# Kernel optimization log

Measured on AMD Instinct MI355X. Metric: run time of the kernel, lower is better.

Reference implementation:

```python
import jax, jax.numpy as jnp
import numpy as np

EPS = 0.5        # epsilon
LAM1 = 1.0       # lambda_1
LAM2 = 1.0       # lambda_2
LAM3 = 0.5       # lambda_3
NLAYER = 2
N, F = 4096, 512


def setup_inputs() -> dict:
    key = jax.random.key(0)
    ks = jax.random.split(key, 7)
    feat = jax.random.normal(ks[0], (N, F), jnp.float32)
    # scale uniform adjacencies by 1/n to mimic normalized Laplacians
    adj = jax.random.uniform(ks[1], (N, N), jnp.float32) / N
    adj1 = jax.random.uniform(ks[2], (N, N), jnp.float32) / N
    y = jax.random.uniform(ks[3], (N, F), jnp.float32)
    wy = jax.random.uniform(ks[4], (F, F), jnp.float32) * 0.01
    lim = 1.0 / np.sqrt(3 * F)
    w2_w = jax.random.uniform(ks[5], (F, 3 * F), jnp.float32, -lim, lim)
    w2_b = jax.random.uniform(ks[6], (F,), jnp.float32, -lim, lim)
    return dict(feat=feat, adj=adj, adj1=adj1, y=y, wy=wy, w2_w=w2_w, w2_b=w2_b)


def _l2norm(x):
    n = jnp.sqrt(jnp.sum(x * x, axis=1, keepdims=True))
    return x / jnp.maximum(n, 1e-12)


def reference(feat, adj, adj1, y, wy, w2_w, w2_b):
    # eval mode: dropout is identity
    z1 = feat
    z2 = feat
    for _ in range(NLAYER):
        yw = y @ wy          # [n,f]
        z1w = z1 @ wy
        z2w = z2 @ wy
        # x @ wy @ wy.T @ x.T == (x@wy) @ (x@wy).T  -> n x n Gram matrices
        temp01 = yw @ yw.T
        temp02 = z1w @ z1w.T
        temp03 = z2w @ z2w.T
        temp11 = temp01 - EPS * temp02 - (1.0 - EPS) * temp03   # [n,n]
        temp12 = yw @ wy.T + (y @ wy.T) @ wy                     # [n,f]
        temp1 = jax.nn.sigmoid(temp11 @ temp12)
        y_n = feat - LAM3 * temp1

        temp21 = -temp11                                         # [n,n]
        temp24 = z1w @ wy.T + (z1 @ wy.T) @ wy                   # [n,f]
        temp2 = jax.nn.sigmoid(temp21 @ temp24)
        z1_n = adj @ z1 - EPS * (LAM3 / LAM1) * temp2

        temp34 = z2w @ wy.T + (z2 @ wy.T) @ wy                   # [n,f]
        temp3 = jax.nn.sigmoid(temp21 @ temp34)
        z2_n = adj1 @ z2 - (1.0 - EPS) * (LAM3 / LAM2) * temp3

        y, z1, z2 = y_n, z1_n, z2_n

    p = jnp.concatenate([_l2norm(y), _l2norm(z1), _l2norm(z2)], axis=1)  # [n,3f]
    logits = p @ w2_w.T + w2_b
    return jax.nn.log_softmax(logits, axis=1)
```

## Files before the change

### kernel.cpp

```cpp
#include <hip/hip_runtime.h>
#include <string.h>

typedef unsigned short u16;
typedef __bf16 bf16_t;
typedef bf16_t bf16x8 __attribute__((ext_vector_type(8)));
typedef float f32x4 __attribute__((ext_vector_type(4)));
typedef u16 u16x4 __attribute__((ext_vector_type(4)));

#define MODE_PLAIN 0
#define MODE_FUSEQT 1
#define MODE_PARTIAL 2
#define MODE_SFIN 3
#define MODE_BIASF32 4

#define SLC 2097152L

__device__ __forceinline__ float bf2f(u16 u) {
  unsigned int x = ((unsigned int)u) << 16;
  return __builtin_bit_cast(float, x);
}
__device__ __forceinline__ u16 f2bf(float f) {
  unsigned int x = __builtin_bit_cast(unsigned int, f);
  x += 0x7fffu + ((x >> 16) & 1u);
  return (u16)(x >> 16);
}

__device__ __forceinline__ void gload_lds16(const void* g, void* l) {
  __builtin_amdgcn_global_load_lds(
      (const __attribute__((address_space(1))) void*)g,
      (__attribute__((address_space(3))) void*)l, 16, 0, 0);
}

struct GemmP {
  const u16* A0; const u16* A1;
  const u16* B;  long bz;
  const float* Bf;
  int lda, ldb, K, ksl, mode;
  u16* C; int ldc;
  u16* XwT; u16* TTp; u16* Pn;
  float* Cf; long cfz; int ldcf;
  const float* Ef; const float* Up; u16* Yc;
  const float* biasf; float* Cff;
};

__global__ __launch_bounds__(256) void gemm_nt(GemmP p) {
  __shared__ u16 smem[2 * 128 * 64];
  const int tid = threadIdx.x;
  const int lane = tid & 63, wave = tid >> 6;
  const int z = blockIdx.z >> p.ksl;
  const int kc = blockIdx.z & ((1 << p.ksl) - 1);
  const long tileM = (long)blockIdx.y * 128;
  const long tileN = (long)blockIdx.x * 128;
  u16* ldsA = smem;
  u16* ldsB = smem + 128 * 64;

  const u16* A = (z == 0) ? p.A0 : p.A1;
  const u16* B = p.B + (long)z * p.bz;
  const float* Bf = p.Bf;

  const int srow = wave * 8 + (lane >> 3);
  const int ssc = lane & 7;
  long aoff[4], boff[4];
#pragma unroll
  for (int j = 0; j < 4; ++j) {
    int r = j * 32 + srow;
    int c = ssc ^ (r & 7);
    aoff[j] = ((tileM + r) * (long)p.lda + c * 8) * 2;
    boff[j] = ((tileN + r) * (long)p.ldb + c * 8) * 2;
  }
  const int frow = tid >> 4, fcol = tid & 15;

  const int r15 = lane & 15, q = lane >> 4;
  const int wm = (wave & 1) * 64, wn = (wave >> 1) * 64;

  f32x4 acc[4][4];
#pragma unroll
  for (int i = 0; i < 4; ++i)
#pragma unroll
    for (int j = 0; j < 4; ++j) { f32x4 zz = {0.f, 0.f, 0.f, 0.f}; acc[i][j] = zz; }

  const int K64 = p.K >> 6;
  const long kofs = (long)kc * K64;
  for (int kt = 0; kt < K64; ++kt) {
    const long kb = (kofs + kt) * 128;
    __syncthreads();
#pragma unroll
    for (int j = 0; j < 4; ++j)
      gload_lds16((const char*)A + aoff[j] + kb, (char*)ldsA + (j * 256 + wave * 64) * 16);
    if (Bf) {
#pragma unroll
      for (int i = 0; i < 8; ++i) {
        int r = i * 16 + frow;
        f32x4 v = *(const f32x4*)(Bf + (tileN + r) * (long)p.ldb + (kofs + kt) * 64 + fcol * 4);
        int sc = (fcol >> 1) ^ (r & 7);
        u16x4 o; o[0] = f2bf(v[0]); o[1] = f2bf(v[1]); o[2] = f2bf(v[2]); o[3] = f2bf(v[3]);
        *(u16x4*)(ldsB + (r * 8 + sc) * 8 + (fcol & 1) * 4) = o;
      }
    } else {
#pragma unroll
      for (int j = 0; j < 4; ++j)
        gload_lds16((const char*)B + boff[j] + kb, (char*)ldsB + (j * 256 + wave * 64) * 16);
    }
    __syncthreads();
#pragma unroll
    for (int ks = 0; ks < 2; ++ks) {
      bf16x8 af[4], bfr[4];
#pragma unroll
      for (int mt = 0; mt < 4; ++mt) {
        int row = wm + mt * 16 + r15;
        int sc = (ks * 4 + q) ^ (r15 & 7);
        af[mt] = *(const bf16x8*)(ldsA + (row * 8 + sc) * 8);
      }
#pragma unroll
      for (int nt = 0; nt < 4; ++nt) {
        int row = wn + nt * 16 + r15;
        int sc = (ks * 4 + q) ^ (r15 & 7);
        bfr[nt] = *(const bf16x8*)(ldsB + (row * 8 + sc) * 8);
      }
#pragma unroll
      for (int mt = 0; mt < 4; ++mt)
#pragma unroll
        for (int nt = 0; nt < 4; ++nt)
          acc[mt][nt] = __builtin_amdgcn_mfma_f32_16x16x32_bf16(af[mt], bfr[nt], acc[mt][nt], 0, 0, 0);
    }
  }

  const int mode = p.mode;
#pragma unroll
  for (int mt = 0; mt < 4; ++mt) {
#pragma unroll
    for (int nt = 0; nt < 4; ++nt) {
      long row0 = tileM + wm + mt * 16 + q * 4;
      long col = tileN + wn + nt * 16 + r15;
      if (mode == MODE_FUSEQT) {
        long bm = row0 >> 12, n0 = row0 & 4095;
        u16x4 ov;
#pragma unroll
        for (int r = 0; r < 4; ++r) ov[r] = f2bf(acc[mt][nt][r]);
        if (col < 512) {
          *(u16x4*)(p.XwT + (bm * 512 + col) * 4096 + n0) = ov;
          float s = (bm == 0) ? 1.f : -0.5f;
          u16* pn = p.Pn + n0 * 1536 + bm * 512 + col;
#pragma unroll
          for (int r = 0; r < 4; ++r) pn[(long)r * 1536] = f2bf(s * acc[mt][nt][r]);
        } else {
          *(u16x4*)(p.TTp + (bm * 512 + (col - 512)) * 4096 + n0) = ov;
        }
      } else if (mode == MODE_PARTIAL) {
        float* c = p.Cf + (long)blockIdx.z * p.cfz + row0 * p.ldcf + col;
#pragma unroll
        for (int r = 0; r < 4; ++r) c[(long)r * p.ldcf] = acc[mt][nt][r];
      } else if (mode == MODE_SFIN) {
        long b = col >> 9, f = col & 511;
#pragma unroll
        for (int r = 0; r < 4; ++r) {
          long row = row0 + r;
          float v = acc[mt][nt][r];
          float o;
          if (b == 0) {
            o = p.Ef[row * 512 + f] - 0.5f * (1.f / (1.f + __expf(-v)));
          } else {
            const float* u = p.Up + (b - 1) * 2 * SLC + row * 512 + f;
            float e = u[0] + u[SLC];
            o = e - 0.25f * (1.f / (1.f + __expf(v)));
          }
          p.Yc[b * SLC + row * 512 + f] = f2bf(o);
        }
      } else if (mode == MODE_BIASF32) {
#pragma unroll
        for (int r = 0; r < 4; ++r)
          p.Cff[(row0 + r) * 512 + col] = acc[mt][nt][r] + p.biasf[col];
      } else {
#pragma unroll
        for (int r = 0; r < 4; ++r)
          p.C[(row0 + r) * (long)p.ldc + col] = f2bf(acc[mt][nt][r]);
      }
    }
  }
}


__global__ __launch_bounds__(256) void pack_m2_k(const float* wy, u16* M2, u16* Bcat) {
  int idx = blockIdx.x * 256 + threadIdx.x;
  int i = idx >> 9, j = idx & 511;
  u16 a = f2bf(wy[idx]);
  u16 b = f2bf(wy[(long)j * 512 + i]);
  M2[(long)i * 1024 + j] = a;
  M2[(long)i * 1024 + 512 + j] = b;
  Bcat[(long)i * 512 + j] = b;
}

__global__ __launch_bounds__(256) void init_ycat_k(const float* y, const float* feat, u16* Ycat) {
  long idx = (long)blockIdx.x * 256 + threadIdx.x;
  f32x4 a = ((const f32x4*)y)[idx];
  f32x4 f = ((const f32x4*)feat)[idx];
  u16x4 ua, uf;
#pragma unroll
  for (int i = 0; i < 4; ++i) { ua[i] = f2bf(a[i]); uf[i] = f2bf(f[i]); }
  ((u16x4*)Ycat)[idx] = ua;
  ((u16x4*)Ycat)[idx + 524288] = uf;
  ((u16x4*)Ycat)[idx + 1048576] = uf;
}

__global__ __launch_bounds__(256) void cvt_adj_k(const float* a0, const float* a1, u16* dst) {
  int z = blockIdx.y;
  const float* src = z ? a1 : a0;
  long idx = (long)blockIdx.x * 256 + threadIdx.x;
  f32x4 v = ((const f32x4*)src)[idx];
  u16x4 o;
#pragma unroll
  for (int i = 0; i < 4; ++i) o[i] = f2bf(v[i]);
  ((u16x4*)(dst + (long)z * 16777216))[idx] = o;
}

__global__ __launch_bounds__(256) void transpose_k(const u16* in, u16* out, long inz, long outz) {
  __shared__ u16 t[64][68];
  const u16* src = in + (long)blockIdx.z * inz;
  u16* dst = out + (long)blockIdx.z * outz;
  int tid = threadIdx.x;
  int tr = tid >> 4, tc = (tid & 15) * 4;
  long r0 = (long)blockIdx.y * 64, c0 = (long)blockIdx.x * 64;
#pragma unroll
  for (int i = 0; i < 4; ++i) {
    int r = i * 16 + tr;
    uint2 v = *(const uint2*)(src + (r0 + r) * 512 + c0 + tc);
    t[r][tc] = (u16)(v.x & 0xffff); t[r][tc + 1] = (u16)(v.x >> 16);
    t[r][tc + 2] = (u16)(v.y & 0xffff); t[r][tc + 3] = (u16)(v.y >> 16);
  }
  __syncthreads();
#pragma unroll
  for (int i = 0; i < 4; ++i) {
    int r = i * 16 + tr;
    unsigned int a0 = t[tc + 0][r], a1 = t[tc + 1][r], a2 = t[tc + 2][r], a3 = t[tc + 3][r];
    uint2 v; v.x = a0 | (a1 << 16); v.y = a2 | (a3 << 16);
    *(uint2*)(dst + (c0 + r) * 4096 + r0 + tc) = v;
  }
}

__global__ __launch_bounds__(256) void wt_reduce_k(const float* Wp, u16* Wt) {
  long idx = (long)blockIdx.x * 256 + threadIdx.x;
  f32x4 s = ((const f32x4*)Wp)[idx];
#pragma unroll
  for (int kc = 1; kc < 4; ++kc) s += ((const f32x4*)Wp)[idx + (long)kc * 589824];
  u16x4 o;
#pragma unroll
  for (int i = 0; i < 4; ++i) o[i] = f2bf(s[i]);
  ((u16x4*)Wt)[idx] = o;
}

__device__ __forceinline__ float waveRedSum(float v) {
#pragma unroll
  for (int o = 32; o > 0; o >>= 1) v += __shfl_down(v, o, 64);
  return v;
}
__device__ __forceinline__ float waveRedMax(float v) {
#pragma unroll
  for (int o = 32; o > 0; o >>= 1) v = fmaxf(v, __shfl_down(v, o, 64));
  return v;
}

__global__ __launch_bounds__(256) void l2norm_k(const u16* Ycat, u16* pb) {
  __shared__ float red[4];
  int i = blockIdx.x, b = blockIdx.y, t = threadIdx.x;
  const u16* row = Ycat + ((long)b * 4096 + (long)i) * 512;
  unsigned int v = *(const unsigned int*)(row + 2 * t);
  float x0 = bf2f((u16)(v & 0xffff)), x1 = bf2f((u16)(v >> 16));
  float w = waveRedSum(x0 * x0 + x1 * x1);
  if ((t & 63) == 0) red[t >> 6] = w;
  __syncthreads();
  float tot = red[0] + red[1] + red[2] + red[3];
  float inv = 1.f / fmaxf(sqrtf(tot), 1e-12f);
  unsigned int o = (unsigned int)f2bf(x0 * inv) | ((unsigned int)f2bf(x1 * inv) << 16);
  *(unsigned int*)(pb + (long)i * 1536 + b * 512 + 2 * t) = o;
}

__global__ __launch_bounds__(256) void logsoftmax_k(const float* lg, float* out) {
  __shared__ float red[4];
  int i = blockIdx.x, t = threadIdx.x;
  const float* row = lg + (long)i * 512;
  float a = row[t], b2 = row[t + 256];
  float m = waveRedMax(fmaxf(a, b2));
  if ((t & 63) == 0) red[t >> 6] = m;
  __syncthreads();
  float M = fmaxf(fmaxf(red[0], red[1]), fmaxf(red[2], red[3]));
  __syncthreads();
  float w = waveRedSum(__expf(a - M) + __expf(b2 - M));
  if ((t & 63) == 0) red[t >> 6] = w;
  __syncthreads();
  float S = red[0] + red[1] + red[2] + red[3];
  float lse = M + __logf(S);
  out[(long)i * 512 + t] = a - lse;
  out[(long)i * 512 + t + 256] = b2 - lse;
}

extern "C" void kernel_launch(void* const* d_in, const int* in_sizes, int n_in,
                              void* d_out, int out_size, void* d_ws, size_t ws_size,
                              hipStream_t stream) {
  const float* feat = (const float*)d_in[0];
  const float* adj  = (const float*)d_in[1];
  const float* adj1 = (const float*)d_in[2];
  const float* y    = (const float*)d_in[3];
  const float* wy   = (const float*)d_in[4];
  const float* w2w  = (const float*)d_in[5];
  const float* w2b  = (const float*)d_in[6];
  (void)in_sizes; (void)n_in; (void)out_size; (void)ws_size;

  char* ws = (char*)d_ws;
  size_t off = 0;
  auto alloc = [&](size_t bytes) -> void* {
    void* r = ws + off; off += (bytes + 255) & ~(size_t)255; return r;
  };
  u16* M2   = (u16*)alloc(512L * 1024 * 2);
  u16* Bcat = (u16*)alloc(1024L * 512 * 2);
  u16* adjb = (u16*)alloc(2L * 4096 * 4096 * 2);
  u16* Ycat = (u16*)alloc(3L * 4096 * 512 * 2);
  u16* Pn   = (u16*)alloc(4096L * 1536 * 2);
  u16* XwT  = (u16*)alloc(3L * 512 * 4096 * 2);
  u16* TT   = (u16*)alloc(3L * 512 * 4096 * 2);
  u16* Zt   = (u16*)alloc(2L * 512 * 4096 * 2);
  u16* Wt   = (u16*)alloc(1536L * 1536 * 2);
  float* WU = (float*)alloc(4L * 1536 * 1536 * 4);
  u16* pb = XwT;
  float* logits = (float*)Zt;

  pack_m2_k<<<1024, 256, 0, stream>>>(wy, M2, Bcat);
  init_ycat_k<<<2048, 256, 0, stream>>>(y, feat, Ycat);
  cvt_adj_k<<<dim3(16384, 2), 256, 0, stream>>>(adj, adj1, adjb);

  { GemmP p = {}; p.A0 = p.A1 = M2; p.B = M2; p.lda = 1024; p.ldb = 1024; p.K = 1024;
    p.mode = MODE_PLAIN; p.C = Bcat + 512L * 512; p.ldc = 512;
    gemm_nt<<<dim3(4, 4, 1), 256, 0, stream>>>(p); }

  for (int L = 0; L < 2; ++L) {
    { GemmP p = {}; p.A0 = p.A1 = Ycat; p.B = Bcat; p.lda = 512; p.ldb = 512; p.K = 512;
      p.mode = MODE_FUSEQT; p.XwT = XwT; p.TTp = TT; p.Pn = Pn;
      gemm_nt<<<dim3(8, 96, 1), 256, 0, stream>>>(p); }
    transpose_k<<<dim3(8, 64, 2), 256, 0, stream>>>(Ycat + SLC, Zt, SLC, SLC);
    { GemmP p = {}; p.A0 = p.A1 = TT; p.B = XwT; p.lda = 4096; p.ldb = 4096;
      p.K = 1024; p.ksl = 2; p.mode = MODE_PARTIAL; p.Cf = WU; p.cfz = 2359296; p.ldcf = 1536;
      gemm_nt<<<dim3(12, 12, 4), 256, 0, stream>>>(p); }
    wt_reduce_k<<<2304, 256, 0, stream>>>(WU, Wt);
    { GemmP p = {}; p.A0 = adjb; p.A1 = adjb + 16777216L; p.B = Zt; p.bz = SLC;
      p.lda = 4096; p.ldb = 4096; p.K = 2048; p.ksl = 1;
      p.mode = MODE_PARTIAL; p.Cf = WU; p.cfz = SLC; p.ldcf = 512;
      gemm_nt<<<dim3(4, 32, 4), 256, 0, stream>>>(p); }
    { GemmP p = {}; p.A0 = p.A1 = Pn; p.B = Wt; p.lda = 1536; p.ldb = 1536; p.K = 1536;
      p.mode = MODE_SFIN; p.Ef = feat; p.Up = WU; p.Yc = Ycat;
      gemm_nt<<<dim3(12, 32, 1), 256, 0, stream>>>(p); }
  }

  l2norm_k<<<dim3(4096, 3, 1), 256, 0, stream>>>(Ycat, pb);
  { GemmP p = {}; p.A0 = p.A1 = pb; p.Bf = w2w; p.lda = 1536; p.ldb = 1536; p.K = 1536;
    p.mode = MODE_BIASF32; p.Cff = logits; p.biasf = w2b;
    gemm_nt<<<dim3(4, 32, 1), 256, 0, stream>>>(p); }
  logsoftmax_k<<<4096, 256, 0, stream>>>(logits, (float*)d_out);
}
```

Measured before the change: 650.2 us.

## Merge independent GEMMs and elementwise jobs into heterogeneous persistent-grid launches

Replaces the per-stage gemm_nt and elementwise kernels with one fused_k kernel that dispatches several independent jobs by block-id range. Adjacency conversion, Ycat init and transposes now share a launch with GEMMs, and the Wt GEMM runs unsplit alongside the adj GEMM, which removes wt_reduce. The final logits GEMM is split-K, and its partials are summed with the bias inside logsoftmax. The aim is fewer launches and better occupancy of small grids, at the cost of imbalanced mixed blocks and a longer serial K loop for Wt.

```diff
diff --git a/kernel.cpp b/kernel.cpp
--- a/kernel.cpp
+++ b/kernel.cpp
@@ -1,5 +1,4 @@
 #include <hip/hip_runtime.h>
-#include <string.h>
 
 typedef unsigned short u16;
 typedef __bf16 bf16_t;
@@ -11,7 +10,9 @@
 #define MODE_FUSEQT 1
 #define MODE_PARTIAL 2
 #define MODE_SFIN 3
-#define MODE_BIASF32 4
+#define MODE_CVT 4
+#define MODE_INIT 5
+#define MODE_TRANS 6
 
 #define SLC 2097152L
 
@@ -31,26 +32,85 @@
       (__attribute__((address_space(3))) void*)l, 16, 0, 0);
 }
 
-struct GemmP {
-  const u16* A0; const u16* A1;
-  const u16* B;  long bz;
-  const float* Bf;
-  int lda, ldb, K, ksl, mode;
-  u16* C; int ldc;
-  u16* XwT; u16* TTp; u16* Pn;
-  float* Cf; long cfz; int ldcf;
-  const float* Ef; const float* Up; u16* Yc;
-  const float* biasf; float* Cff;
+struct Job {
+  int mode, gx, gy, ksl;
+  const u16 *A0, *A1, *B; long bz;
+  const float *Bf;
+  int lda, ldb, K;
+  u16 *C; long cfz; int ldc;
+  u16 *XwT, *TTp, *Pn;
+  float *Cf; int ldcf;
+  const float *Ef, *Up; u16 *Yc;
+  const float *S0, *S1; u16 *D0;
 };
-
-__global__ __launch_bounds__(256) void gemm_nt(GemmP p) {
-  __shared__ u16 smem[2 * 128 * 64];
+struct LaunchP { Job j[3]; int s1, s2; };
+
+__device__ __forceinline__ void run_job(const Job& p, int rb, u16* smem) {
   const int tid = threadIdx.x;
+
+  if (p.mode == MODE_CVT) {
+    const float* src = (rb < 256) ? p.S0 : p.S1;
+    u16* dst = p.D0 + ((rb < 256) ? 0L : 16777216L);
+    int r = rb & 255;
+#pragma unroll 4
+    for (int i = 0; i < 64; ++i) {
+      long idx = (long)i * 65536 + r * 256 + tid;
+      f32x4 v = ((const f32x4*)src)[idx];
+      u16x4 o;
+#pragma unroll
+      for (int k = 0; k < 4; ++k) o[k] = f2bf(v[k]);
+      ((u16x4*)dst)[idx] = o;
+    }
+    return;
+  }
+  if (p.mode == MODE_INIT) {
+#pragma unroll
+    for (int i = 0; i < 8; ++i) {
+      long idx = (long)i * 65536 + rb * 256 + tid;
+      f32x4 a = ((const f32x4*)p.S0)[idx];
+      f32x4 f = ((const f32x4*)p.S1)[idx];
+      u16x4 ua, uf;
+#pragma unroll
+      for (int k = 0; k < 4; ++k) { ua[k] = f2bf(a[k]); uf[k] = f2bf(f[k]); }
+      ((u16x4*)p.D0)[idx] = ua;
+      ((u16x4*)p.D0)[idx + 524288] = uf;
+      ((u16x4*)p.D0)[idx + 1048576] = uf;
+    }
+    return;
+  }
+  if (p.mode == MODE_TRANS) {
+    u16 (*t)[68] = (u16(*)[68])smem;
+    int zi = rb >> 9, rem = rb & 511;
+    int bx = rem >> 6, by = rem & 63;
+    const u16* src = p.A0 + (long)zi * p.bz;
+    u16* dst = p.C + (long)zi * p.cfz;
+    int tr = tid >> 4, tc = (tid & 15) * 4;
+    long r0 = (long)by * 64, c0 = (long)bx * 64;
+#pragma unroll
+    for (int i = 0; i < 4; ++i) {
+      int r = i * 16 + tr;
+      uint2 v = *(const uint2*)(src + (r0 + r) * 512 + c0 + tc);
+      t[r][tc] = (u16)(v.x & 0xffff); t[r][tc + 1] = (u16)(v.x >> 16);
+      t[r][tc + 2] = (u16)(v.y & 0xffff); t[r][tc + 3] = (u16)(v.y >> 16);
+    }
+    __syncthreads();
+#pragma unroll
+    for (int i = 0; i < 4; ++i) {
+      int r = i * 16 + tr;
+      unsigned int a0 = t[tc + 0][r], a1 = t[tc + 1][r], a2 = t[tc + 2][r], a3 = t[tc + 3][r];
+      uint2 v; v.x = a0 | (a1 << 16); v.y = a2 | (a3 << 16);
+      *(uint2*)(dst + (c0 + r) * 4096 + r0 + tc) = v;
+    }
+    return;
+  }
+
   const int lane = tid & 63, wave = tid >> 6;
-  const int z = blockIdx.z >> p.ksl;
-  const int kc = blockIdx.z & ((1 << p.ksl) - 1);
-  const long tileM = (long)blockIdx.y * 128;
-  const long tileN = (long)blockIdx.x * 128;
+  int per = p.gx * p.gy;
+  int zi = rb / per, rem = rb - zi * per;
+  int bx = rem / p.gy, by = rem - bx * p.gy;
+  int z = zi >> p.ksl, kc = zi & ((1 << p.ksl) - 1);
+  const long tileM = (long)by * 128;
+  const long tileN = (long)bx * 128;
   u16* ldsA = smem;
   u16* ldsB = smem + 128 * 64;
 
@@ -147,7 +207,7 @@
           *(u16x4*)(p.TTp + (bm * 512 + (col - 512)) * 4096 + n0) = ov;
         }
       } else if (mode == MODE_PARTIAL) {
-        float* c = p.Cf + (long)blockIdx.z * p.cfz + row0 * p.ldcf + col;
+        float* c = p.Cf + (long)zi * p.cfz + row0 * p.ldcf + col;
 #pragma unroll
         for (int r = 0; r < 4; ++r) c[(long)r * p.ldcf] = acc[mt][nt][r];
       } else if (mode == MODE_SFIN) {
@@ -166,10 +226,6 @@
           }
           p.Yc[b * SLC + row * 512 + f] = f2bf(o);
         }
-      } else if (mode == MODE_BIASF32) {
-#pragma unroll
-        for (int r = 0; r < 4; ++r)
-          p.Cff[(row0 + r) * 512 + col] = acc[mt][nt][r] + p.biasf[col];
       } else {
 #pragma unroll
         for (int r = 0; r < 4; ++r)
@@ -177,6 +233,14 @@
       }
     }
   }
+}
+
+__global__ __launch_bounds__(256) void fused_k(LaunchP lp) {
+  __shared__ u16 smem[2 * 128 * 64];
+  int bid = blockIdx.x;
+  if (bid < lp.s1) run_job(lp.j[0], bid, smem);
+  else if (bid < lp.s2) run_job(lp.j[1], bid - lp.s1, smem);
+  else run_job(lp.j[2], bid - lp.s2, smem);
 }
 
 
@@ -188,64 +252,6 @@
   M2[(long)i * 1024 + j] = a;
   M2[(long)i * 1024 + 512 + j] = b;
   Bcat[(long)i * 512 + j] = b;
-}
-
-__global__ __launch_bounds__(256) void init_ycat_k(const float* y, const float* feat, u16* Ycat) {
-  long idx = (long)blockIdx.x * 256 + threadIdx.x;
-  f32x4 a = ((const f32x4*)y)[idx];
-  f32x4 f = ((const f32x4*)feat)[idx];
-  u16x4 ua, uf;
-#pragma unroll
-  for (int i = 0; i < 4; ++i) { ua[i] = f2bf(a[i]); uf[i] = f2bf(f[i]); }
-  ((u16x4*)Ycat)[idx] = ua;
-  ((u16x4*)Ycat)[idx + 524288] = uf;
-  ((u16x4*)Ycat)[idx + 1048576] = uf;
-}
-
-__global__ __launch_bounds__(256) void cvt_adj_k(const float* a0, const float* a1, u16* dst) {
-  int z = blockIdx.y;
-  const float* src = z ? a1 : a0;
-  long idx = (long)blockIdx.x * 256 + threadIdx.x;
-  f32x4 v = ((const f32x4*)src)[idx];
-  u16x4 o;
-#pragma unroll
-  for (int i = 0; i < 4; ++i) o[i] = f2bf(v[i]);
-  ((u16x4*)(dst + (long)z * 16777216))[idx] = o;
-}
-
-__global__ __launch_bounds__(256) void transpose_k(const u16* in, u16* out, long inz, long outz) {
-  __shared__ u16 t[64][68];
-  const u16* src = in + (long)blockIdx.z * inz;
-  u16* dst = out + (long)blockIdx.z * outz;
-  int tid = threadIdx.x;
-  int tr = tid >> 4, tc = (tid & 15) * 4;
-  long r0 = (long)blockIdx.y * 64, c0 = (long)blockIdx.x * 64;
-#pragma unroll
-  for (int i = 0; i < 4; ++i) {
-    int r = i * 16 + tr;
-    uint2 v = *(const uint2*)(src + (r0 + r) * 512 + c0 + tc);
-    t[r][tc] = (u16)(v.x & 0xffff); t[r][tc + 1] = (u16)(v.x >> 16);
-    t[r][tc + 2] = (u16)(v.y & 0xffff); t[r][tc + 3] = (u16)(v.y >> 16);
-  }
-  __syncthreads();
-#pragma unroll
-  for (int i = 0; i < 4; ++i) {
-    int r = i * 16 + tr;
-    unsigned int a0 = t[tc + 0][r], a1 = t[tc + 1][r], a2 = t[tc + 2][r], a3 = t[tc + 3][r];
-    uint2 v; v.x = a0 | (a1 << 16); v.y = a2 | (a3 << 16);
-    *(uint2*)(dst + (c0 + r) * 4096 + r0 + tc) = v;
-  }
-}
-
-__global__ __launch_bounds__(256) void wt_reduce_k(const float* Wp, u16* Wt) {
-  long idx = (long)blockIdx.x * 256 + threadIdx.x;
-  f32x4 s = ((const f32x4*)Wp)[idx];
-#pragma unroll
-  for (int kc = 1; kc < 4; ++kc) s += ((const f32x4*)Wp)[idx + (long)kc * 589824];
-  u16x4 o;
-#pragma unroll
-  for (int i = 0; i < 4; ++i) o[i] = f2bf(s[i]);
-  ((u16x4*)Wt)[idx] = o;
 }
 
 __device__ __forceinline__ float waveRedSum(float v) {
@@ -274,11 +280,12 @@
   *(unsigned int*)(pb + (long)i * 1536 + b * 512 + 2 * t) = o;
 }
 
-__global__ __launch_bounds__(256) void logsoftmax_k(const float* lg, float* out) {
+__global__ __launch_bounds__(256) void logsoftmax_k(const float* lg, const float* bias, float* out) {
   __shared__ float red[4];
   int i = blockIdx.x, t = threadIdx.x;
   const float* row = lg + (long)i * 512;
-  float a = row[t], b2 = row[t + 256];
+  float a  = row[t]       + row[t + SLC]       + row[t + 2 * SLC]       + row[t + 3 * SLC]       + bias[t];
+  float b2 = row[t + 256] + row[t + 256 + SLC] + row[t + 256 + 2 * SLC] + row[t + 256 + 3 * SLC] + bias[t + 256];
   float m = waveRedMax(fmaxf(a, b2));
   if ((t & 63) == 0) red[t >> 6] = m;
   __syncthreads();
@@ -319,39 +326,60 @@
   u16* TT   = (u16*)alloc(3L * 512 * 4096 * 2);
   u16* Zt   = (u16*)alloc(2L * 512 * 4096 * 2);
   u16* Wt   = (u16*)alloc(1536L * 1536 * 2);
-  float* WU = (float*)alloc(4L * 1536 * 1536 * 4);
+  float* WU = (float*)alloc(4L * SLC * 4);
   u16* pb = XwT;
-  float* logits = (float*)Zt;
 
   pack_m2_k<<<1024, 256, 0, stream>>>(wy, M2, Bcat);
-  init_ycat_k<<<2048, 256, 0, stream>>>(y, feat, Ycat);
-  cvt_adj_k<<<dim3(16384, 2), 256, 0, stream>>>(adj, adj1, adjb);
-
-  { GemmP p = {}; p.A0 = p.A1 = M2; p.B = M2; p.lda = 1024; p.ldb = 1024; p.K = 1024;
-    p.mode = MODE_PLAIN; p.C = Bcat + 512L * 512; p.ldc = 512;
-    gemm_nt<<<dim3(4, 4, 1), 256, 0, stream>>>(p); }
+
+  { LaunchP lp = {};
+    Job& a = lp.j[0]; a.mode = MODE_PLAIN; a.gx = 4; a.gy = 4; a.K = 1024;
+    a.A0 = a.A1 = M2; a.B = M2; a.lda = 1024; a.ldb = 1024;
+    a.C = Bcat + 512L * 512; a.ldc = 512;
+    Job& b = lp.j[1]; b.mode = MODE_INIT; b.S0 = y; b.S1 = feat; b.D0 = Ycat;
+    lp.s1 = 16; lp.s2 = 272;
+    fused_k<<<272, 256, 0, stream>>>(lp); }
 
   for (int L = 0; L < 2; ++L) {
-    { GemmP p = {}; p.A0 = p.A1 = Ycat; p.B = Bcat; p.lda = 512; p.ldb = 512; p.K = 512;
-      p.mode = MODE_FUSEQT; p.XwT = XwT; p.TTp = TT; p.Pn = Pn;
-      gemm_nt<<<dim3(8, 96, 1), 256, 0, stream>>>(p); }
-    transpose_k<<<dim3(8, 64, 2), 256, 0, stream>>>(Ycat + SLC, Zt, SLC, SLC);
-    { GemmP p = {}; p.A0 = p.A1 = TT; p.B = XwT; p.lda = 4096; p.ldb = 4096;
-      p.K = 1024; p.ksl = 2; p.mode = MODE_PARTIAL; p.Cf = WU; p.cfz = 2359296; p.ldcf = 1536;
-      gemm_nt<<<dim3(12, 12, 4), 256, 0, stream>>>(p); }
-    wt_reduce_k<<<2304, 256, 0, stream>>>(WU, Wt);
-    { GemmP p = {}; p.A0 = adjb; p.A1 = adjb + 16777216L; p.B = Zt; p.bz = SLC;
-      p.lda = 4096; p.ldb = 4096; p.K = 2048; p.ksl = 1;
-      p.mode = MODE_PARTIAL; p.Cf = WU; p.cfz = SLC; p.ldcf = 512;
-      gemm_nt<<<dim3(4, 32, 4), 256, 0, stream>>>(p); }
-    { GemmP p = {}; p.A0 = p.A1 = Pn; p.B = Wt; p.lda = 1536; p.ldb = 1536; p.K = 1536;
-      p.mode = MODE_SFIN; p.Ef = feat; p.Up = WU; p.Yc = Ycat;
-      gemm_nt<<<dim3(12, 32, 1), 256, 0, stream>>>(p); }
+    { LaunchP lp = {};
+      Job& a = lp.j[0]; a.mode = MODE_FUSEQT; a.gx = 8; a.gy = 96; a.K = 512;
+      a.A0 = a.A1 = Ycat; a.B = Bcat; a.lda = 512; a.ldb = 512;
+      a.XwT = XwT; a.TTp = TT; a.Pn = Pn;
+      Job& b = lp.j[1]; b.mode = MODE_TRANS; b.A0 = Ycat + SLC; b.bz = SLC;
+      b.C = Zt; b.cfz = SLC;
+      int grid = 1792;
+      lp.s1 = 768; lp.s2 = 1792;
+      if (L == 0) {
+        Job& c = lp.j[2]; c.mode = MODE_CVT; c.S0 = adj; c.S1 = adj1; c.D0 = adjb;
+        grid = 2304;
+      }
+      fused_k<<<grid, 256, 0, stream>>>(lp); }
+
+    { LaunchP lp = {};
+      Job& a = lp.j[0]; a.mode = MODE_PARTIAL; a.gx = 4; a.gy = 32; a.ksl = 1; a.K = 2048;
+      a.A0 = adjb; a.A1 = adjb + 16777216L; a.B = Zt; a.bz = SLC;
+      a.lda = 4096; a.ldb = 4096; a.Cf = WU; a.cfz = SLC; a.ldcf = 512;
+      Job& b = lp.j[1]; b.mode = MODE_PLAIN; b.gx = 12; b.gy = 12; b.K = 4096;
+      b.A0 = b.A1 = TT; b.B = XwT; b.lda = 4096; b.ldb = 4096;
+      b.C = Wt; b.ldc = 1536;
+      lp.s1 = 512; lp.s2 = 656;
+      fused_k<<<656, 256, 0, stream>>>(lp); }
+
+    { LaunchP lp = {};
+      Job& a = lp.j[0]; a.mode = MODE_SFIN; a.gx = 12; a.gy = 32; a.K = 1536;
+      a.A0 = a.A1 = Pn; a.B = Wt; a.lda = 1536; a.ldb = 1536;
+      a.Ef = feat; a.Up = WU; a.Yc = Ycat;
+      lp.s1 = 384; lp.s2 = 384;
+      fused_k<<<384, 256, 0, stream>>>(lp); }
   }
 
   l2norm_k<<<dim3(4096, 3, 1), 256, 0, stream>>>(Ycat, pb);
-  { GemmP p = {}; p.A0 = p.A1 = pb; p.Bf = w2w; p.lda = 1536; p.ldb = 1536; p.K = 1536;
-    p.mode = MODE_BIASF32; p.Cff = logits; p.biasf = w2b;
-    gemm_nt<<<dim3(4, 32, 1), 256, 0, stream>>>(p); }
-  logsoftmax_k<<<4096, 256, 0, stream>>>(logits, (float*)d_out);
-}
+
+  { LaunchP lp = {};
+    Job& a = lp.j[0]; a.mode = MODE_PARTIAL; a.gx = 4; a.gy = 32; a.ksl = 2; a.K = 384;
+    a.A0 = a.A1 = pb; a.Bf = w2w; a.lda = 1536; a.ldb = 1536;
+    a.Cf = WU; a.cfz = SLC; a.ldcf = 512;
+    lp.s1 = 512; lp.s2 = 512;
+    fused_k<<<512, 256, 0, stream>>>(lp); }
+
+  logsoftmax_k<<<4096, 256, 0, stream>>>(WU, w2b, (float*)d_out);
+}
```

Result: faster. 637.3 us (-2.0%).
